# Optimization experiments

Measured on AMD Instinct MI355X. Metric: run time of the kernel, lower is better.

The kernel has to match this reference:

```python
import jax, jax.numpy as jnp
import numpy as np

ALPHA = 0.1  # dt/tau = 10/100


def setup_inputs() -> dict:
    key = jax.random.key(0)
    k1, k2, k3 = jax.random.split(key, 3)
    seq_len, batch, in_dim, hid = 1024, 64, 128, 512
    inp = jax.random.normal(k1, (seq_len, batch, in_dim), dtype=jnp.float32)
    W_in = jax.random.normal(k2, (hid, in_dim), dtype=jnp.float32) / np.sqrt(in_dim)
    b_in = jnp.zeros((hid,), dtype=jnp.float32)
    W_hid = jax.random.normal(k3, (hid, hid), dtype=jnp.float32) / np.sqrt(hid)
    b_hid = jnp.zeros((hid,), dtype=jnp.float32)
    return {"input": inp, "W_in": W_in, "b_in": b_in, "W_hid": W_hid, "b_hid": b_hid}


def reference(input, W_in, b_in, W_hid, b_hid):
    # leaky RNN: v_t = (1-a) v_{t-1} + a (W_hid fr_{t-1} + b_hid + W_in u_t + b_in)
    #            fr_t = relu(v_t)
    hid = W_hid.shape[0]
    batch = input.shape[1]
    # precompute input projection for all steps: (seq, batch, hid)
    u_proj = jnp.einsum('sbi,hi->sbh', input, W_in) + b_in

    v0 = jnp.zeros((batch, hid), dtype=input.dtype)
    fr0 = jax.nn.relu(v0)

    def step(carry, u_t):
        fr, v = carry
        v = (1.0 - ALPHA) * v + ALPHA * (fr @ W_hid.T + b_hid + u_t)
        fr = jax.nn.relu(v)
        return (fr, v), fr

    _, states = jax.lax.scan(step, (fr0, v0), u_proj)
    return states  # (seq_len, batch, hidden)
```

## Files before the change

### kernel.cpp

```cpp
#include <hip/hip_runtime.h>
#include <hip/hip_bf16.h>
#include <stdint.h>


#define SEQ   1024
#define BATCH 64
#define INDIM 128
#define HID   512
#define HG    16
#define BGN   4
#define SXS   20

typedef __attribute__((ext_vector_type(8))) short   short8;
typedef __attribute__((ext_vector_type(4))) float   floatx4;
typedef unsigned long long ull;

__device__ __forceinline__ unsigned short f2bf(float x) {
  union { float f; unsigned int u; } v; v.f = x;
  unsigned int r = v.u + 0x7fffu + ((v.u >> 16) & 1u);
  return (unsigned short)(r >> 16);
}
__device__ __forceinline__ ull pack4(unsigned short a, unsigned short b,
                                     unsigned short c, unsigned short d) {
  return (ull)a | ((ull)b << 16) | ((ull)c << 32) | ((ull)d << 48);
}

#define TA_SB 64
#define TA_H  128
#define TA_K  64
#define APAD  65

__global__ __launch_bounds__(256) void uproj_kernel(
    const float* __restrict__ inp, const float* __restrict__ Win,
    const float* __restrict__ bin, float* __restrict__ out)
{
  __shared__ float sIn[TA_SB * APAD];
  __shared__ float sW [TA_H  * APAD];
  const int tid = threadIdx.x;
  const int sb0 = (blockIdx.x >> 2) * TA_SB;
  const int h0  = (blockIdx.x & 3) * TA_H;
  const int tx = tid & 15, ty = tid >> 4;

  float acc[4][8];
  #pragma unroll
  for (int i = 0; i < 4; ++i)
    #pragma unroll
    for (int j = 0; j < 8; ++j) acc[i][j] = 0.f;

  for (int kt = 0; kt < INDIM / TA_K; ++kt) {
    #pragma unroll
    for (int p = 0; p < 4; ++p) {
      int idx = tid + 256 * p;
      int row = idx >> 4, c4 = (idx & 15) << 2;
      const float4 v = *(const float4*)(inp + (size_t)(sb0 + row) * INDIM + kt * TA_K + c4);
      float* d = sIn + row * APAD + c4;
      d[0] = v.x; d[1] = v.y; d[2] = v.z; d[3] = v.w;
    }
    #pragma unroll
    for (int p = 0; p < 8; ++p) {
      int idx = tid + 256 * p;
      int row = idx >> 4, c4 = (idx & 15) << 2;
      const float4 v = *(const float4*)(Win + (size_t)(h0 + row) * INDIM + kt * TA_K + c4);
      float* d = sW + row * APAD + c4;
      d[0] = v.x; d[1] = v.y; d[2] = v.z; d[3] = v.w;
    }
    __syncthreads();

    for (int k = 0; k < TA_K; ++k) {
      float a[4], b[8];
      #pragma unroll
      for (int i = 0; i < 4; ++i) a[i] = sIn[(ty + 16 * i) * APAD + k];
      #pragma unroll
      for (int j = 0; j < 8; ++j) b[j] = sW[(tx + 16 * j) * APAD + k];
      #pragma unroll
      for (int i = 0; i < 4; ++i)
        #pragma unroll
        for (int j = 0; j < 8; ++j) acc[i][j] = fmaf(a[i], b[j], acc[i][j]);
    }
    __syncthreads();
  }

  #pragma unroll
  for (int j = 0; j < 8; ++j) {
    float bb = bin[h0 + tx + 16 * j];
    #pragma unroll
    for (int i = 0; i < 4; ++i)
      out[(size_t)(sb0 + ty + 16 * i) * HID + h0 + tx + 16 * j] = acc[i][j] + bb;
  }
}

__global__ __launch_bounds__(128) void scan_kernel(
    const float* __restrict__ Whid, const float* __restrict__ bhid,
    float* __restrict__ uo,
    ull* __restrict__ frA)
{
  __shared__ unsigned short sX[32 * SXS];

  const int tid  = threadIdx.x;
  const int lane = tid & 63;
  const int wave = tid >> 6;
  const int bg = blockIdx.x >> 4;
  const int hg = blockIdx.x & 15;
  const int b0 = bg * 16;
  const int h0 = hg * 32;

  const int cn = lane & 15;
  const int q  = lane >> 4;
  const int mq = q * 4;
  const int nl = wave * 16 + cn;
  const int ng = h0 + nl;
  const float bias = bhid[ng];

  short8 bw[HG];
  {
    const float* wrow = Whid + (size_t)ng * HID + q * 8;
    #pragma unroll
    for (int kk = 0; kk < HG; ++kk) {
      const float4 a = *(const float4*)(wrow + kk * 32);
      const float4 b = *(const float4*)(wrow + kk * 32 + 4);
      union { unsigned short s[8]; short8 v; } u;
      u.s[0] = f2bf(a.x); u.s[1] = f2bf(a.y); u.s[2] = f2bf(a.z); u.s[3] = f2bf(a.w);
      u.s[4] = f2bf(b.x); u.s[5] = f2bf(b.y); u.s[6] = f2bf(b.z); u.s[7] = f2bf(b.w);
      bw[kk] = u.v;
    }
  }

  const int pl  = tid >> 1, ph = tid & 1;
  const int pm  = pl & 15;
  const int pk0 = (pl >> 4) * 8 + ph * 4;

  const ull MASKT = 0x8000800080008000ull;
  float v[4] = {0.f, 0.f, 0.f, 0.f};
  const float OMA = 0.9f, AL = 0.1f;

  for (int t = 0; t < SEQ; ++t) {
    const float* up = uo + ((size_t)t * BATCH + b0 + mq) * HID + ng;
    float uu[4];
    #pragma unroll
    for (int r = 0; r < 4; ++r) uu[r] = up[(size_t)r * HID];

    floatx4 acc[4];
    #pragma unroll
    for (int j = 0; j < 4; ++j) acc[j] = (floatx4){0.f, 0.f, 0.f, 0.f};

    if (t > 0) {
      const int slot = (t - 1) & 1;
      const ull expv = (((t - 1) >> 1) & 1) ? MASKT : 0ull;
      const ull* ap = frA + (size_t)(slot * BGN + bg) * HG * 128 + (size_t)lane * 2;
      ull lo[HG], hi[HG];
      for (;;) {
        int ok = 1;
        #pragma unroll
        for (int kk = 0; kk < HG; ++kk) {
          lo[kk] = __hip_atomic_load(ap + (size_t)kk * 128,
                                     __ATOMIC_RELAXED, __HIP_MEMORY_SCOPE_AGENT);
          hi[kk] = __hip_atomic_load(ap + (size_t)kk * 128 + 1,
                                     __ATOMIC_RELAXED, __HIP_MEMORY_SCOPE_AGENT);
          ok &= (int)(((lo[kk] & MASKT) == expv) & ((hi[kk] & MASKT) == expv));
        }
        if (__all(ok)) break;
      }
      #pragma unroll
      for (int kk = 0; kk < HG; ++kk) {
        union { ull u[2]; short8 s; } af;
        af.u[0] = lo[kk] & ~MASKT;
        af.u[1] = hi[kk] & ~MASKT;
        acc[kk & 3] = __builtin_amdgcn_mfma_f32_16x16x32_bf16(af.s, bw[kk],
                                                              acc[kk & 3], 0, 0, 0);
      }
    }

    float fr[4];
    #pragma unroll
    for (int r = 0; r < 4; ++r) {
      float s = acc[0][r] + acc[1][r] + acc[2][r] + acc[3][r];
      v[r] = OMA * v[r] + AL * (s + bias + uu[r]);
      fr[r] = fmaxf(v[r], 0.f);
    }

    *(ull*)(sX + nl * SXS + mq) = pack4(f2bf(fr[0]), f2bf(fr[1]),
                                        f2bf(fr[2]), f2bf(fr[3]));
    __syncthreads();
    {
      unsigned short g0 = sX[(pk0 + 0) * SXS + pm];
      unsigned short g1 = sX[(pk0 + 1) * SXS + pm];
      unsigned short g2 = sX[(pk0 + 2) * SXS + pm];
      unsigned short g3 = sX[(pk0 + 3) * SXS + pm];
      ull pk = pack4(g0, g1, g2, g3);
      if ((t >> 1) & 1) pk |= MASKT;
      ull* dst = frA + (size_t)(((t & 1) * BGN + bg) * HG + hg) * 128
                     + (size_t)pl * 2 + ph;
      __hip_atomic_store(dst, pk, __ATOMIC_RELAXED, __HIP_MEMORY_SCOPE_AGENT);
    }

    float* op = uo + ((size_t)t * BATCH + b0 + mq) * HID + ng;
    #pragma unroll
    for (int r = 0; r < 4; ++r) op[(size_t)r * HID] = fr[r];

    __syncthreads();
  }
}

extern "C" void kernel_launch(void* const* d_in, const int* in_sizes, int n_in,
                              void* d_out, int out_size, void* d_ws, size_t ws_size,
                              hipStream_t stream) {
  const float* inp  = (const float*)d_in[0];
  const float* Win  = (const float*)d_in[1];
  const float* bin  = (const float*)d_in[2];
  const float* Whid = (const float*)d_in[3];
  const float* bhid = (const float*)d_in[4];
  float* out = (float*)d_out;

  ull* frA = (ull*)d_ws;

  uproj_kernel<<<dim3((65536 / TA_SB) * (HID / TA_H)), dim3(256), 0, stream>>>(
      inp, Win, bin, out);
  scan_kernel<<<dim3(BGN * HG), dim3(128), 0, stream>>>(
      Whid, bhid, out, frA);
}
```

Baseline: 2.354 ms.

## Swap MFMA operands so each wave publishes its own state without LDS transpose

The recurrent scan now puts the weights in the MFMA A operand and the previous state in B, so each lane's output already has the layout the next step's consumers expect. The shared-memory transpose and both block barriers per step go away. Each block becomes a single 64-thread wave, and the grid doubles to 128 blocks. The u-projection read and the output write become float4 accesses, at the cost of more blocks polling the global flags.

New measurement: 2.152 ms. 8.6% less time.

```diff
diff --git a/kernel.cpp b/kernel.cpp
--- a/kernel.cpp
+++ b/kernel.cpp
@@ -9,7 +9,6 @@
 #define HID   512
 #define HG    16
 #define BGN   4
-#define SXS   20
 
 typedef __attribute__((ext_vector_type(8))) short   short8;
 typedef __attribute__((ext_vector_type(4))) float   floatx4;
@@ -89,31 +88,25 @@
   }
 }
 
-__global__ __launch_bounds__(128) void scan_kernel(
+__global__ __launch_bounds__(64) void scan_kernel(
     const float* __restrict__ Whid, const float* __restrict__ bhid,
     float* __restrict__ uo,
     ull* __restrict__ frA)
 {
-  __shared__ unsigned short sX[32 * SXS];
+  const int lane = threadIdx.x & 63;
+  const int bid  = blockIdx.x;
+  const int bg = bid >> 5;
+  const int hg = (bid >> 1) & 15;
+  const int w  = bid & 1;
+  const int b0 = bg * 16;
+  const int m  = lane & 15;
+  const int q  = lane >> 4;
+  const int n0 = hg * 32 + w * 16 + q * 4;
+  const int na = hg * 32 + w * 16 + m;
 
-  const int tid  = threadIdx.x;
-  const int lane = tid & 63;
-  const int wave = tid >> 6;
-  const int bg = blockIdx.x >> 4;
-  const int hg = blockIdx.x & 15;
-  const int b0 = bg * 16;
-  const int h0 = hg * 32;
-
-  const int cn = lane & 15;
-  const int q  = lane >> 4;
-  const int mq = q * 4;
-  const int nl = wave * 16 + cn;
-  const int ng = h0 + nl;
-  const float bias = bhid[ng];
-
-  short8 bw[HG];
+  short8 aw[HG];
   {
-    const float* wrow = Whid + (size_t)ng * HID + q * 8;
+    const float* wrow = Whid + (size_t)na * HID + q * 8;
     #pragma unroll
     for (int kk = 0; kk < HG; ++kk) {
       const float4 a = *(const float4*)(wrow + kk * 32);
@@ -121,23 +114,17 @@
       union { unsigned short s[8]; short8 v; } u;
       u.s[0] = f2bf(a.x); u.s[1] = f2bf(a.y); u.s[2] = f2bf(a.z); u.s[3] = f2bf(a.w);
       u.s[4] = f2bf(b.x); u.s[5] = f2bf(b.y); u.s[6] = f2bf(b.z); u.s[7] = f2bf(b.w);
-      bw[kk] = u.v;
+      aw[kk] = u.v;
     }
   }
-
-  const int pl  = tid >> 1, ph = tid & 1;
-  const int pm  = pl & 15;
-  const int pk0 = (pl >> 4) * 8 + ph * 4;
+  const floatx4 bias4 = *(const floatx4*)(bhid + n0);
 
   const ull MASKT = 0x8000800080008000ull;
   float v[4] = {0.f, 0.f, 0.f, 0.f};
   const float OMA = 0.9f, AL = 0.1f;
 
   for (int t = 0; t < SEQ; ++t) {
-    const float* up = uo + ((size_t)t * BATCH + b0 + mq) * HID + ng;
-    float uu[4];
-    #pragma unroll
-    for (int r = 0; r < 4; ++r) uu[r] = up[(size_t)r * HID];
+    const floatx4 uu = *(const floatx4*)(uo + ((size_t)t * BATCH + b0 + m) * HID + n0);
 
     floatx4 acc[4];
     #pragma unroll
@@ -146,7 +133,8 @@
     if (t > 0) {
       const int slot = (t - 1) & 1;
       const ull expv = (((t - 1) >> 1) & 1) ? MASKT : 0ull;
-      const ull* ap = frA + (size_t)(slot * BGN + bg) * HG * 128 + (size_t)lane * 2;
+      const ull* ap = frA + (size_t)(slot * BGN + bg) * HG * 128
+                          + (size_t)(2 * q) * 16 + m;
       ull lo[HG], hi[HG];
       for (;;) {
         int ok = 1;
@@ -154,7 +142,7 @@
         for (int kk = 0; kk < HG; ++kk) {
           lo[kk] = __hip_atomic_load(ap + (size_t)kk * 128,
                                      __ATOMIC_RELAXED, __HIP_MEMORY_SCOPE_AGENT);
-          hi[kk] = __hip_atomic_load(ap + (size_t)kk * 128 + 1,
+          hi[kk] = __hip_atomic_load(ap + (size_t)kk * 128 + 16,
                                      __ATOMIC_RELAXED, __HIP_MEMORY_SCOPE_AGENT);
           ok &= (int)(((lo[kk] & MASKT) == expv) & ((hi[kk] & MASKT) == expv));
         }
@@ -162,10 +150,10 @@
       }
       #pragma unroll
       for (int kk = 0; kk < HG; ++kk) {
-        union { ull u[2]; short8 s; } af;
-        af.u[0] = lo[kk] & ~MASKT;
-        af.u[1] = hi[kk] & ~MASKT;
-        acc[kk & 3] = __builtin_amdgcn_mfma_f32_16x16x32_bf16(af.s, bw[kk],
+        union { ull u[2]; short8 s; } bf;
+        bf.u[0] = lo[kk] & ~MASKT;
+        bf.u[1] = hi[kk] & ~MASKT;
+        acc[kk & 3] = __builtin_amdgcn_mfma_f32_16x16x32_bf16(aw[kk], bf.s,
                                                               acc[kk & 3], 0, 0, 0);
       }
     }
@@ -174,30 +162,20 @@
     #pragma unroll
     for (int r = 0; r < 4; ++r) {
       float s = acc[0][r] + acc[1][r] + acc[2][r] + acc[3][r];
-      v[r] = OMA * v[r] + AL * (s + bias + uu[r]);
+      v[r] = OMA * v[r] + AL * (s + bias4[r] + uu[r]);
       fr[r] = fmaxf(v[r], 0.f);
     }
 
-    *(ull*)(sX + nl * SXS + mq) = pack4(f2bf(fr[0]), f2bf(fr[1]),
-                                        f2bf(fr[2]), f2bf(fr[3]));
-    __syncthreads();
     {
-      unsigned short g0 = sX[(pk0 + 0) * SXS + pm];
-      unsigned short g1 = sX[(pk0 + 1) * SXS + pm];
-      unsigned short g2 = sX[(pk0 + 2) * SXS + pm];
-      unsigned short g3 = sX[(pk0 + 3) * SXS + pm];
-      ull pk = pack4(g0, g1, g2, g3);
+      ull pk = pack4(f2bf(fr[0]), f2bf(fr[1]), f2bf(fr[2]), f2bf(fr[3]));
       if ((t >> 1) & 1) pk |= MASKT;
       ull* dst = frA + (size_t)(((t & 1) * BGN + bg) * HG + hg) * 128
-                     + (size_t)pl * 2 + ph;
+                     + (size_t)(w * 4 + q) * 16 + m;
       __hip_atomic_store(dst, pk, __ATOMIC_RELAXED, __HIP_MEMORY_SCOPE_AGENT);
     }
 
-    float* op = uo + ((size_t)t * BATCH + b0 + mq) * HID + ng;
-    #pragma unroll
-    for (int r = 0; r < 4; ++r) op[(size_t)r * HID] = fr[r];
-
-    __syncthreads();
+    *(floatx4*)(uo + ((size_t)t * BATCH + b0 + m) * HID + n0) =
+        (floatx4){fr[0], fr[1], fr[2], fr[3]};
   }
 }
 
@@ -215,6 +193,6 @@
 
   uproj_kernel<<<dim3((65536 / TA_SB) * (HID / TA_H)), dim3(256), 0, stream>>>(
       inp, Win, bin, out);
-  scan_kernel<<<dim3(BGN * HG), dim3(128), 0, stream>>>(
+  scan_kernel<<<dim3(BGN * HG * 2), dim3(64), 0, stream>>>(
       Whid, bhid, out, frA);
 }
```
